# Performance work log

Hardware: AMD Instinct MI355X
Metric: run time of the kernel (lower is better)

Reference implementation:

```python
import jax, jax.numpy as jnp
import numpy as np

HEADS = 8
DIM = 512
DIM_HEAD = 64          # dim // 8
LANDMARKS = 256        # dim // 2
PINV_ITERS = 6
KSIZE = 33             # residual depthwise conv kernel (lucidrains default)
LN_EPS = 1e-5


def setup_inputs() -> dict:
    key = jax.random.key(0)
    ks = jax.random.split(key, 5)
    b, n, d = 4, 4096, DIM
    inner = HEADS * DIM_HEAD  # 512
    x = jax.random.normal(ks[0], (b, n, d), jnp.float32)
    w_qkv = jax.random.normal(ks[1], (d, inner * 3), jnp.float32) * 0.02   # to_qkv (no bias)
    w_out = jax.random.normal(ks[2], (inner, d), jnp.float32) * 0.02      # to_out linear
    b_out = jnp.zeros((d,), jnp.float32)
    res_kernel = jax.random.normal(ks[3], (HEADS, 1, KSIZE, 1), jnp.float32) * 0.02  # depthwise Conv2d, groups=heads, no bias
    gamma = jnp.ones((d,), jnp.float32)
    beta = jnp.zeros((d,), jnp.float32)
    return dict(x=x, w_qkv=w_qkv, w_out=w_out, b_out=b_out,
                res_kernel=res_kernel, gamma=gamma, beta=beta)


def _moore_penrose_pinv(mat, iters):
    # Faithful to lucidrains moore_penrose_iter_pinv: global-max scaling init.
    abs_m = jnp.abs(mat)
    col = abs_m.sum(-1)
    row = abs_m.sum(-2)
    z = jnp.swapaxes(mat, -1, -2) / (jnp.max(col) * jnp.max(row))
    eye = jnp.eye(mat.shape[-1], dtype=mat.dtype)
    for _ in range(iters):
        mz = mat @ z
        z = 0.25 * z @ (13.0 * eye - mz @ (15.0 * eye - mz @ (7.0 * eye - mz)))
    return z


def reference(x, w_qkv, w_out, b_out, res_kernel, gamma, beta):
    b, n, d = x.shape
    # --- pre-norm (torch LayerNorm: biased variance) ---
    mu = x.mean(-1, keepdims=True)
    var = ((x - mu) ** 2).mean(-1, keepdims=True)
    xn = (x - mu) / jnp.sqrt(var + LN_EPS) * gamma + beta

    # --- qkv ---
    qkv = xn @ w_qkv                                     # [b, n, 3*inner]
    q, k, v = jnp.split(qkv, 3, axis=-1)
    split = lambda t: t.reshape(b, n, HEADS, DIM_HEAD).transpose(0, 2, 1, 3)  # [b,h,n,d]
    q, k, v = split(q), split(k), split(v)
    q = q * (DIM_HEAD ** -0.5)

    # --- landmarks (n divisible by LANDMARKS: no padding branch) ---
    m = LANDMARKS
    l = n // m
    q_l = q.reshape(b, HEADS, m, l, DIM_HEAD).mean(3)    # [b,h,m,d]
    k_l = k.reshape(b, HEADS, m, l, DIM_HEAD).mean(3)

    attn1 = jax.nn.softmax(jnp.einsum('bhid,bhjd->bhij', q, k_l), axis=-1)   # [b,h,n,m]
    attn2 = jax.nn.softmax(jnp.einsum('bhid,bhjd->bhij', q_l, k_l), axis=-1) # [b,h,m,m]
    attn3 = jax.nn.softmax(jnp.einsum('bhid,bhjd->bhij', q_l, k), axis=-1)   # [b,h,m,n]
    attn2_inv = _moore_penrose_pinv(attn2, PINV_ITERS)

    out = (attn1 @ attn2_inv) @ (attn3 @ v)              # [b,h,n,d]

    # --- depthwise conv residual over sequence dim (groups=heads) ---
    pad = KSIZE // 2
    res = jax.lax.conv_general_dilated(
        v, res_kernel, window_strides=(1, 1), padding=((pad, pad), (0, 0)),
        dimension_numbers=('NCHW', 'OIHW', 'NCHW'), feature_group_count=HEADS)
    out = out + res

    # --- merge heads, output proj (dropout = identity at inference) ---
    out = out.transpose(0, 2, 1, 3).reshape(b, n, HEADS * DIM_HEAD)
    out = out @ w_out + b_out

    # --- outer residual ---
    return x + out
```

## Files before the change

kernel.cpp:

```cpp
#include <hip/hip_runtime.h>
#include <stdint.h>

#define DEV __device__ __forceinline__

typedef unsigned short u16;
typedef unsigned int u32;
using f32x4 = __attribute__((ext_vector_type(4))) float;
using u32x4 = __attribute__((ext_vector_type(4))) u32;
using bf16x8 = __attribute__((ext_vector_type(8))) __bf16;

DEV float b2f(u16 u) { u32 x = ((u32)u) << 16; return __builtin_bit_cast(float, x); }
DEV u16 f2b(float f) {
  u32 x = __builtin_bit_cast(u32, f);
  return (u16)((x + 0x7FFFu + ((x >> 16) & 1u)) >> 16);
}
DEV u32 pk2(float a, float b) { return (u32)f2b(a) | ((u32)f2b(b) << 16); }
DEV bf16x8 lds_frag(const u16* p) { return __builtin_bit_cast(bf16x8, *(const u32x4*)p); }
DEV bf16x8 g_frag(const u16* p) { return __builtin_bit_cast(bf16x8, *(const u32x4*)p); }
DEV f32x4 mfma16(bf16x8 a, bf16x8 b, f32x4 c) {
  return __builtin_amdgcn_mfma_f32_16x16x32_bf16(a, b, c, 0, 0, 0);
}
DEV float wredmax(float v) {
#pragma unroll
  for (int m = 32; m > 0; m >>= 1) v = fmaxf(v, __shfl_xor(v, m));
  return v;
}
DEV float wredsum(float v) {
#pragma unroll
  for (int m = 32; m > 0; m >>= 1) v += __shfl_xor(v, m);
  return v;
}

__global__ __launch_bounds__(256) void ln_k(const float* __restrict__ x,
                                            const float* __restrict__ gamma,
                                            const float* __restrict__ beta,
                                            u16* __restrict__ xn) {
  int row = blockIdx.x, tid = threadIdx.x;
  int lane = tid & 63, wave = tid >> 6;
  const float* xr = x + (size_t)row * 512;
  float a = xr[2 * tid], b = xr[2 * tid + 1];
  __shared__ float red[8];
  float s = wredsum(a + b);
  if (lane == 0) red[wave] = s;
  __syncthreads();
  float mean = (red[0] + red[1] + red[2] + red[3]) * (1.0f / 512.0f);
  float da = a - mean, db = b - mean;
  float vs = wredsum(da * da + db * db);
  if (lane == 0) red[4 + wave] = vs;
  __syncthreads();
  float var = (red[4] + red[5] + red[6] + red[7]) * (1.0f / 512.0f);
  float rstd = rsqrtf(var + 1e-5f);
  int c = 2 * tid;
  u16 o0 = f2b(da * rstd * gamma[c] + beta[c]);
  u16 o1 = f2b(db * rstd * gamma[c + 1] + beta[c + 1]);
  *(u32*)&xn[(size_t)row * 512 + c] = (u32)o0 | ((u32)o1 << 16);
}

__global__ __launch_bounds__(256) void transpose_w(const float* __restrict__ in,
                                                   u16* __restrict__ out, int R, int C) {
  __shared__ float t[64][65];
  int c0 = blockIdx.x * 64, r0 = blockIdx.y * 64;
  int tid = threadIdx.x;
  int r = tid >> 2, cs = (tid & 3) * 16;
  const float* src = in + (size_t)(r0 + r) * C + c0 + cs;
#pragma unroll
  for (int e = 0; e < 16; e++) t[r][cs + e] = src[e];
  __syncthreads();
  int c = tid >> 2, rs = (tid & 3) * 16;
  u16* dst = out + (size_t)(c0 + c) * R + r0 + rs;
#pragma unroll
  for (int e = 0; e < 16; e++) dst[e] = f2b(t[rs + e][c]);
}

__global__ __launch_bounds__(256) void transpose_k(const u16* __restrict__ k,
                                                   u16* __restrict__ kT) {
  __shared__ u16 t[64][72];
  int bh = blockIdx.y, i0 = blockIdx.x * 64;
  int tid = threadIdx.x;
  int r = tid >> 2, ds = (tid & 3) * 16;
  const u16* src = k + (((size_t)bh * 4096) + i0 + r) * 64 + ds;
#pragma unroll
  for (int e = 0; e < 16; e++) t[r][ds + e] = src[e];
  __syncthreads();
  int d = tid >> 2, is = (tid & 3) * 16;
  u16* dst = kT + ((size_t)bh * 64 + d) * 4096 + i0 + is;
#pragma unroll
  for (int e = 0; e < 16; e++) dst[e] = t[is + e][d];
}

__global__ __launch_bounds__(256) void landmark_mean(const u16* __restrict__ src,
                                                     u16* __restrict__ dh,
                                                     u16* __restrict__ dl,
                                                     u16* __restrict__ dF) {
  int gid = blockIdx.x * 4 + (threadIdx.x >> 6);
  int lane = threadIdx.x & 63;
  int bh = gid >> 8, lm = gid & 255;
  const u16* p = src + (((size_t)bh * 4096) + lm * 16) * 64 + lane;
  float s = 0.f;
#pragma unroll
  for (int t = 0; t < 16; t++) s += b2f(p[t * 64]);
  float m = s * (1.0f / 16.0f);
  u16 hi = f2b(m);
  size_t idx = ((size_t)bh * 256 + lm) * 64 + lane;
  dh[idx] = hi;
  dl[idx] = f2b(m - b2f(hi));
  if (dF) {
    size_t a = ((((size_t)bh * 16 + (lm >> 4)) * 2 + (lane >> 5)) * 512) +
               (((lane >> 3) & 3) * 128) + ((lm & 15) * 8) + (lane & 7);
    dF[a] = hi;
  }
}

template <int MODE>
__global__ __launch_bounds__(256) void gemm_bf16_nt(
    const u16* __restrict__ A, const u16* __restrict__ Bt, int K,
    u16* __restrict__ oq, u16* __restrict__ ok, u16* __restrict__ ov,
    const float* __restrict__ xres, const float* __restrict__ bias,
    float* __restrict__ oc) {
  constexpr int BM = 128, BN = 128, BK = 32, LDT = BK + 8;
  constexpr int SMEM = (MODE == 1) ? (128 * 132 * 4) : (128 * 136 * 2);
  __shared__ __align__(16) char smem[SMEM];
  u16(*Al)[LDT] = (u16(*)[LDT])smem;
  u16(*Bl)[LDT] = (u16(*)[LDT])(smem + BM * LDT * 2);
  int tid = threadIdx.x;
  int lane = tid & 63, wave = tid >> 6;
  int bm = blockIdx.x * BM, bn = blockIdx.y * BN;
  int wm = (wave >> 1) * 64, wn = (wave & 1) * 64;
  f32x4 acc[4][4] = {};
  for (int kt = 0; kt < K; kt += BK) {
    __syncthreads();
#pragma unroll
    for (int c = 0; c < 2; c++) {
      int chunk = tid + c * 256;
      int r = chunk >> 2, kc = (chunk & 3) * 8;
      const u16* src;
      if (MODE == 0) {
        src = A + (size_t)(bm + r) * K + kt + kc;
      } else {
        int m = bm + r, kk = kt + kc;
        src = A + ((((size_t)(m >> 12)) * 8 + (kk >> 6)) * 4096 + (m & 4095)) * 64 + (kk & 63);
      }
      *(u32x4*)&Al[r][kc] = *(const u32x4*)src;
      const u16* srcb = Bt + (size_t)(bn + r) * K + kt + kc;
      *(u32x4*)&Bl[r][kc] = *(const u32x4*)srcb;
    }
    __syncthreads();
    bf16x8 af[4], bf_[4];
#pragma unroll
    for (int i = 0; i < 4; i++) af[i] = lds_frag(&Al[wm + i * 16 + (lane & 15)][8 * (lane >> 4)]);
#pragma unroll
    for (int i = 0; i < 4; i++) bf_[i] = lds_frag(&Bl[wn + i * 16 + (lane & 15)][8 * (lane >> 4)]);
#pragma unroll
    for (int mi = 0; mi < 4; mi++)
#pragma unroll
      for (int ni = 0; ni < 4; ni++) acc[mi][ni] = mfma16(af[mi], bf_[ni], acc[mi][ni]);
  }
  __syncthreads();
  if (MODE == 0) {
    u16(*Cl)[136] = (u16(*)[136])smem;
    int tensor = bn / 512;
    float scale = (tensor == 0) ? 0.125f : 1.0f;
#pragma unroll
    for (int mi = 0; mi < 4; mi++)
      for (int ni = 0; ni < 4; ni++)
        for (int r = 0; r < 4; r++) {
          int row = wm + mi * 16 + 4 * (lane >> 4) + r;
          int col = wn + ni * 16 + (lane & 15);
          Cl[row][col] = f2b(acc[mi][ni][r] * scale);
        }
    __syncthreads();
    int half = tid >> 7, r = tid & 127;
    int m = bm + r, b = m >> 12, i = m & 4095;
    int cw = (bn % 512) + half * 64;
    int h = cw >> 6;
    u16* base = (tensor == 0) ? oq : (tensor == 1 ? ok : ov);
    u16* dst = base + (((size_t)(b * 8 + h)) * 4096 + i) * 64;
#pragma unroll
    for (int j = 0; j < 64; j += 8) *(u32x4*)(dst + j) = *(const u32x4*)&Cl[r][half * 64 + j];
  } else {
    float(*Cf)[132] = (float(*)[132])smem;
#pragma unroll
    for (int mi = 0; mi < 4; mi++)
      for (int ni = 0; ni < 4; ni++)
        for (int r = 0; r < 4; r++) {
          int row = wm + mi * 16 + 4 * (lane >> 4) + r;
          int col = wn + ni * 16 + (lane & 15);
          Cf[row][col] = acc[mi][ni][r];
        }
    __syncthreads();
    int r = tid >> 1, seg = (tid & 1) * 64;
    int m = bm + r;
    const float* xr = xres + (size_t)m * 512 + bn + seg;
    const float* br = bias + bn + seg;
    float* orow = oc + (size_t)m * 512 + bn + seg;
#pragma unroll
    for (int j = 0; j < 64; j += 4) {
      f32x4 cv = *(const f32x4*)&Cf[r][seg + j];
      f32x4 xv = *(const f32x4*)&xr[j];
      f32x4 bv = *(const f32x4*)&br[j];
      cv = cv + xv + bv;
      *(f32x4*)&orow[j] = cv;
    }
  }
}

template <int OMODE, int PREC>
__global__ __launch_bounds__(256) void ns_gemm(
    const u16* __restrict__ Ahg, const u16* __restrict__ Alg,
    const u16* __restrict__ Bhg, const u16* __restrict__ Blg, int K, int sA, int sB,
    u16* __restrict__ Ch, u16* __restrict__ Cl2, u16* __restrict__ Th, u16* __restrict__ Tl,
    float* __restrict__ Cf, u16* __restrict__ Tu,
    float cC, float aC, float cT, float aT, int wrC, int wrT) {
  __shared__ __align__(16) u16 Ahs[64][72], Als[64][72], Bhs[64][72], Bls[64][72];
  int bz = blockIdx.z;
  int tid = threadIdx.x, lane = tid & 63, wave = tid >> 6;
  int l15 = lane & 15, g = lane >> 4;
  int bm = blockIdx.x * 64, bn = blockIdx.y * 64;
  int wm = (wave >> 1) * 32, wn = (wave & 1) * 32;
  const u16* Ah0 = Ahg + (size_t)bz * sA;
  const u16* Al0 = Alg + (size_t)bz * sA;
  const u16* Bh0 = Bhg + (size_t)bz * sB;
  const u16* Bl0 = Blg + (size_t)bz * sB;
  int r = tid >> 2, c16 = (tid & 3) * 16;
  const u16* pa = Ah0 + (size_t)(bm + r) * K + c16;
  const u16* pal = Al0 + (size_t)(bm + r) * K + c16;
  const u16* pb = Bh0 + (size_t)(bn + r) * K + c16;
  const u16* pbl = Bl0 + (size_t)(bn + r) * K + c16;
  u32x4 ra0 = *(const u32x4*)pa, ra1 = *(const u32x4*)(pa + 8);
  u32x4 rc0 = *(const u32x4*)pb, rc1 = *(const u32x4*)(pb + 8);
  u32x4 rb0, rb1, rd0, rd1;
  if (PREC) {
    rb0 = *(const u32x4*)pal;
    rb1 = *(const u32x4*)(pal + 8);
    rd0 = *(const u32x4*)pbl;
    rd1 = *(const u32x4*)(pbl + 8);
  }
  f32x4 acc[2][2] = {};
  int nt = K >> 6;
  for (int t = 0; t < nt; t++) {
    __syncthreads();
    *(u32x4*)&Ahs[r][c16] = ra0;
    *(u32x4*)&Ahs[r][c16 + 8] = ra1;
    *(u32x4*)&Bhs[r][c16] = rc0;
    *(u32x4*)&Bhs[r][c16 + 8] = rc1;
    if (PREC) {
      *(u32x4*)&Als[r][c16] = rb0;
      *(u32x4*)&Als[r][c16 + 8] = rb1;
      *(u32x4*)&Bls[r][c16] = rd0;
      *(u32x4*)&Bls[r][c16 + 8] = rd1;
    }
    __syncthreads();
    if (t + 1 < nt) {
      int kt = (t + 1) << 6;
      ra0 = *(const u32x4*)(pa + kt);
      ra1 = *(const u32x4*)(pa + kt + 8);
      rc0 = *(const u32x4*)(pb + kt);
      rc1 = *(const u32x4*)(pb + kt + 8);
      if (PREC) {
        rb0 = *(const u32x4*)(pal + kt);
        rb1 = *(const u32x4*)(pal + kt + 8);
        rd0 = *(const u32x4*)(pbl + kt);
        rd1 = *(const u32x4*)(pbl + kt + 8);
      }
    }
#pragma unroll
    for (int ks = 0; ks < 2; ks++) {
      int ko = ks * 32 + 8 * g;
      bf16x8 ah[2], al[2], bh_[2], bl_[2];
#pragma unroll
      for (int i = 0; i < 2; i++) {
        int ro = wm + i * 16 + l15;
        int rn = wn + i * 16 + l15;
        ah[i] = lds_frag(&Ahs[ro][ko]);
        bh_[i] = lds_frag(&Bhs[rn][ko]);
        if (PREC) {
          al[i] = lds_frag(&Als[ro][ko]);
          bl_[i] = lds_frag(&Bls[rn][ko]);
        }
      }
#pragma unroll
      for (int mi = 0; mi < 2; mi++)
#pragma unroll
        for (int ni = 0; ni < 2; ni++) {
          acc[mi][ni] = mfma16(ah[mi], bh_[ni], acc[mi][ni]);
          if (PREC) {
            acc[mi][ni] = mfma16(ah[mi], bl_[ni], acc[mi][ni]);
            acc[mi][ni] = mfma16(al[mi], bh_[ni], acc[mi][ni]);
          }
        }
    }
  }
#pragma unroll
  for (int mi = 0; mi < 2; mi++)
#pragma unroll
    for (int ni = 0; ni < 2; ni++) {
      int r0 = bm + wm + mi * 16 + 4 * g;
      int cg = bn + wn + ni * 16 + l15;
      f32x4 a = acc[mi][ni];
      if (OMODE == 1) {
        float* c = Cf + (size_t)bz * 65536;
#pragma unroll
        for (int rr = 0; rr < 4; rr++)
          c[(size_t)(r0 + rr) * 256 + cg] = aC * a[rr] + ((r0 + rr) == cg ? cC : 0.f);
      } else if (OMODE == 2) {
        u16 pp[4];
#pragma unroll
        for (int rr = 0; rr < 4; rr++) pp[rr] = f2b(aT * a[rr]);
        u16* tp = Tu + ((((size_t)bz * 4 + (cg >> 4)) * 8 + (r0 >> 5)) * 512) +
                  (((r0 >> 3) & 3) * 128) + ((cg & 15) * 8) + (r0 & 7);
        *(u32*)tp = (u32)pp[0] | ((u32)pp[1] << 16);
        *(u32*)(tp + 2) = (u32)pp[2] | ((u32)pp[3] << 16);
      } else {
        if (wrC) {
#pragma unroll
          for (int rr = 0; rr < 4; rr++) {
            float v = aC * a[rr] + ((r0 + rr) == cg ? cC : 0.f);
            u16 hi = f2b(v);
            size_t idx = (size_t)bz * 65536 + (size_t)(r0 + rr) * 256 + cg;
            Ch[idx] = hi;
            Cl2[idx] = f2b(v - b2f(hi));
          }
        }
        if (wrT) {
          u16 ph[4], pl[4];
#pragma unroll
          for (int rr = 0; rr < 4; rr++) {
            float v = aT * a[rr] + ((r0 + rr) == cg ? cT : 0.f);
            ph[rr] = f2b(v);
            pl[rr] = f2b(v - b2f(ph[rr]));
          }
          size_t idx = (size_t)bz * 65536 + (size_t)cg * 256 + r0;
          *(u32*)&Th[idx] = (u32)ph[0] | ((u32)ph[1] << 16);
          *(u32*)&Th[idx + 2] = (u32)ph[2] | ((u32)ph[3] << 16);
          *(u32*)&Tl[idx] = (u32)pl[0] | ((u32)pl[1] << 16);
          *(u32*)&Tl[idx + 2] = (u32)pl[2] | ((u32)pl[3] << 16);
        }
      }
    }
}

__global__ __launch_bounds__(256) void softmax256(float* __restrict__ S,
                                                  u16* __restrict__ Sh,
                                                  u16* __restrict__ Sl) {
  int row = blockIdx.x * 4 + (threadIdx.x >> 6);
  int lane = threadIdx.x & 63;
  float* r = S + (size_t)row * 256;
  f32x4 vv = *(f32x4*)&r[lane * 4];
  float mx = wredmax(fmaxf(fmaxf(vv[0], vv[1]), fmaxf(vv[2], vv[3])));
  vv[0] = __expf(vv[0] - mx);
  vv[1] = __expf(vv[1] - mx);
  vv[2] = __expf(vv[2] - mx);
  vv[3] = __expf(vv[3] - mx);
  float sm = wredsum(vv[0] + vv[1] + vv[2] + vv[3]);
  vv *= (1.0f / sm);
  *(f32x4*)&r[lane * 4] = vv;
  u16 h[4], l[4];
#pragma unroll
  for (int e = 0; e < 4; e++) {
    h[e] = f2b(vv[e]);
    l[e] = f2b(vv[e] - b2f(h[e]));
  }
  size_t p = (size_t)row * 256 + lane * 4;
  *(u32*)&Sh[p] = (u32)h[0] | ((u32)h[1] << 16);
  *(u32*)&Sh[p + 2] = (u32)h[2] | ((u32)h[3] << 16);
  *(u32*)&Sl[p] = (u32)l[0] | ((u32)l[1] << 16);
  *(u32*)&Sl[p + 2] = (u32)l[2] | ((u32)l[3] << 16);
}

__global__ __launch_bounds__(256) void pinv_part(const float* __restrict__ mat,
                                                 float* __restrict__ colpart,
                                                 float* __restrict__ scal) {
  int blk = blockIdx.x;
  int bh = blk >> 3, ch = blk & 7;
  const float* m = mat + (size_t)bh * 65536 + (size_t)ch * 32 * 256;
  int tid = threadIdx.x, lane = tid & 63, wv = tid >> 6;
  float cp = 0.f;
#pragma unroll 4
  for (int r2 = 0; r2 < 32; r2++) cp += m[r2 * 256 + tid];
  colpart[(size_t)blk * 256 + tid] = cp;
  float rmax = 0.f;
#pragma unroll
  for (int rr = 0; rr < 8; rr++) {
    f32x4 v = *(const f32x4*)&m[(wv * 8 + rr) * 256 + lane * 4];
    float s = wredsum(v[0] + v[1] + v[2] + v[3]);
    rmax = fmaxf(rmax, s);
  }
  if (lane == 0) atomicMax((int*)&scal[1], __float_as_int(rmax));
}

__global__ __launch_bounds__(256) void pinv_fin(const float* __restrict__ colpart,
                                                float* __restrict__ scal) {
  int tid = threadIdx.x;
  float mx = 0.f;
  for (int bh = 0; bh < 32; bh++) {
    float s = 0.f;
#pragma unroll
    for (int ch = 0; ch < 8; ch++) s += colpart[((size_t)bh * 8 + ch) * 256 + tid];
    mx = fmaxf(mx, s);
  }
  mx = wredmax(mx);
  __shared__ float red[4];
  if ((tid & 63) == 0) red[tid >> 6] = mx;
  __syncthreads();
  if (tid == 0) {
    float a = fmaxf(fmaxf(red[0], red[1]), fmaxf(red[2], red[3]));
    atomicMax((int*)&scal[0], __float_as_int(a));
  }
}

__global__ __launch_bounds__(256) void pinv_init(const float* __restrict__ mat,
                                                 const float* __restrict__ scal,
                                                 u16* __restrict__ zh, u16* __restrict__ zl,
                                                 u16* __restrict__ zth, u16* __restrict__ ztl) {
  size_t idx = (size_t)blockIdx.x * 256 + threadIdx.x;
  int bh = (int)(idx >> 16);
  int i = (int)((idx >> 8) & 255), j = (int)(idx & 255);
  float s = 1.0f / (scal[0] * scal[1]);
  float val = mat[idx] * s;
  u16 hi = f2b(val);
  u16 lo = f2b(val - b2f(hi));
  zth[idx] = hi;
  ztl[idx] = lo;
  size_t tixd = ((size_t)bh << 16) + ((size_t)j << 8) + i;
  zh[tixd] = hi;
  zl[tixd] = lo;
}

__global__ __launch_bounds__(512) void attn3_split(const u16* __restrict__ qlh,
                                                   const u16* __restrict__ k,
                                                   const u16* __restrict__ vT,
                                                   float* __restrict__ pacc,
                                                   float* __restrict__ ml) {
  __shared__ __align__(16) u16 kb[64][72];
  __shared__ __align__(16) u16 vtb[64][72];
  __shared__ __align__(16) u16 Pb[8][16][72];
  int tid = threadIdx.x, lane = tid & 63, wv = tid >> 6;
  int l15 = lane & 15, g = lane >> 4;
  int bh = blockIdx.y, kvc = blockIdx.x;
  const u16* kb_g = k + ((size_t)bh * 4096 + (size_t)kvc * 512) * 64;
  const u16* vb_g = vT + (size_t)bh * 64 * 4096 + (size_t)kvc * 512;
  bf16x8 aq[2][2];
#pragma unroll
  for (int ss = 0; ss < 2; ss++) {
    const u16* qlp = qlh + ((size_t)bh * 256 + wv * 32 + ss * 16 + l15) * 64 + 8 * g;
    aq[ss][0] = g_frag(qlp);
    aq[ss][1] = g_frag(qlp + 32);
  }
  int sr = tid >> 3, sc = (tid & 7) * 8;
  u32x4 rk = *(const u32x4*)(kb_g + (size_t)sr * 64 + sc);
  u32x4 rv = *(const u32x4*)(vb_g + (size_t)sr * 4096 + sc);
  f32x4 minit = {-1e30f, -1e30f, -1e30f, -1e30f};
  f32x4 mreg[2] = {minit, minit};
  f32x4 lreg[2] = {};
  f32x4 oacc[2][4] = {};
  for (int t = 0; t < 8; t++) {
    __syncthreads();
    *(u32x4*)&kb[sr][sc] = rk;
    *(u32x4*)&vtb[sr][sc] = rv;
    __syncthreads();
    if (t < 7) {
      rk = *(const u32x4*)(kb_g + (size_t)(t + 1) * 4096 + (size_t)sr * 64 + sc);
      rv = *(const u32x4*)(vb_g + (size_t)(t + 1) * 64 + (size_t)sr * 4096 + sc);
    }
#pragma unroll
    for (int ss = 0; ss < 2; ss++) {
      f32x4 sa[4] = {};
#pragma unroll
      for (int nf = 0; nf < 4; nf++) {
        bf16x8 b0 = lds_frag(&kb[nf * 16 + l15][8 * g]);
        bf16x8 b1 = lds_frag(&kb[nf * 16 + l15][8 * g + 32]);
        sa[nf] = mfma16(aq[ss][0], b0, sa[nf]);
        sa[nf] = mfma16(aq[ss][1], b1, sa[nf]);
      }
      f32x4 mn, corr;
#pragma unroll
      for (int r = 0; r < 4; r++) {
        float m_ = fmaxf(fmaxf(sa[0][r], sa[1][r]), fmaxf(sa[2][r], sa[3][r]));
#pragma unroll
        for (int msk = 1; msk < 16; msk <<= 1) m_ = fmaxf(m_, __shfl_xor(m_, msk));
        mn[r] = fmaxf(mreg[ss][r], m_);
        corr[r] = __expf(mreg[ss][r] - mn[r]);
        mreg[ss][r] = mn[r];
      }
      f32x4 ps = {};
#pragma unroll
      for (int nf = 0; nf < 4; nf++)
#pragma unroll
        for (int r = 0; r < 4; r++) {
          sa[nf][r] = __expf(sa[nf][r] - mn[r]);
          ps[r] += sa[nf][r];
        }
#pragma unroll
      for (int r = 0; r < 4; r++) {
#pragma unroll
        for (int msk = 1; msk < 16; msk <<= 1) ps[r] += __shfl_xor(ps[r], msk);
        lreg[ss][r] = lreg[ss][r] * corr[r] + ps[r];
      }
#pragma unroll
      for (int nf = 0; nf < 4; nf++) oacc[ss][nf] *= corr;
#pragma unroll
      for (int nf = 0; nf < 4; nf++)
#pragma unroll
        for (int r = 0; r < 4; r++)
          Pb[wv][4 * g + r][nf * 16 + l15] = f2b(sa[nf][r]);
      asm volatile("s_waitcnt lgkmcnt(0)" ::: "memory");
      __builtin_amdgcn_sched_barrier(0);
      bf16x8 ap0 = lds_frag(&Pb[wv][l15][8 * g]);
      bf16x8 ap1 = lds_frag(&Pb[wv][l15][8 * g + 32]);
#pragma unroll
      for (int nf = 0; nf < 4; nf++) {
        bf16x8 b0 = lds_frag(&vtb[nf * 16 + l15][8 * g]);
        bf16x8 b1 = lds_frag(&vtb[nf * 16 + l15][8 * g + 32]);
        oacc[ss][nf] = mfma16(ap0, b0, oacc[ss][nf]);
        oacc[ss][nf] = mfma16(ap1, b1, oacc[ss][nf]);
      }
    }
  }
  size_t pb = (size_t)(bh * 8 + kvc) * 64;
#pragma unroll
  for (int ss = 0; ss < 2; ss++) {
    int qbase = wv * 32 + ss * 16;
#pragma unroll
    for (int nf = 0; nf < 4; nf++)
      *(f32x4*)&pacc[(pb + nf * 16 + l15) * 256 + qbase + 4 * g] = oacc[ss][nf];
    if (l15 == 0) {
#pragma unroll
      for (int r = 0; r < 4; r++) {
        size_t mi = ((size_t)(bh * 8 + kvc) * 256 + qbase + 4 * g + r) * 2;
        ml[mi] = mreg[ss][r];
        ml[mi + 1] = lreg[ss][r];
      }
    }
  }
}

__global__ __launch_bounds__(256) void attn3_fin(const float* __restrict__ pacc,
                                                 const float* __restrict__ ml,
                                                 u16* __restrict__ w3h,
                                                 u16* __restrict__ w3l) {
  int dc = blockIdx.x, bh = blockIdx.y;
  int i = threadIdx.x;
  float m[8], l[8], w[8];
  float M = -1e30f;
#pragma unroll
  for (int kv = 0; kv < 8; kv++) {
    size_t mi = ((size_t)(bh * 8 + kv) * 256 + i) * 2;
    m[kv] = ml[mi];
    l[kv] = ml[mi + 1];
    M = fmaxf(M, m[kv]);
  }
  float den = 0.f;
#pragma unroll
  for (int kv = 0; kv < 8; kv++) {
    w[kv] = __expf(m[kv] - M);
    den += w[kv] * l[kv];
  }
  float inv = 1.0f / den;
#pragma unroll
  for (int dd = 0; dd < 16; dd++) {
    int d = dc * 16 + dd;
    float num = 0.f;
#pragma unroll
    for (int kv = 0; kv < 8; kv++)
      num += w[kv] * pacc[((size_t)(bh * 8 + kv) * 64 + d) * 256 + i];
    float val = num * inv;
    u16 hi = f2b(val);
    size_t o = ((size_t)bh * 64 + d) * 256 + i;
    w3h[o] = hi;
    w3l[o] = f2b(val - b2f(hi));
  }
}

__global__ __launch_bounds__(256, 4) void attn1_mfma(const u16* __restrict__ q,
                                                     const u16* __restrict__ kF,
                                                     const u16* __restrict__ zwF,
                                                     const u16* __restrict__ vT,
                                                     const float* __restrict__ rker,
                                                     u16* __restrict__ out_h) {
  __shared__ __align__(16) u16 Pl[64][258];
  int tid = threadIdx.x, lane = tid & 63, wv = tid >> 6;
  int l15 = lane & 15, g = lane >> 4;
  int bh = blockIdx.y, h = bh & 7;
  int i0 = blockIdx.x * 64;
  const u16* qp = q + ((size_t)bh * 4096 + i0 + wv * 16 + l15) * 64 + 8 * g;
  bf16x8 aq0 = __builtin_bit_cast(bf16x8, *(const u32x4*)qp);
  bf16x8 aq1 = __builtin_bit_cast(bf16x8, *(const u32x4*)(qp + 32));
  u16 kb16 = (lane < 33) ? f2b(rker[h * 33 + lane]) : (u16)0;
  const u16* kfb = kF + (size_t)bh * 16384 + (size_t)lane * 8;
  f32x4 sacc[16] = {};
#pragma unroll
  for (int nf = 0; nf < 16; nf++) {
    bf16x8 b0 = g_frag(kfb + (nf * 2 + 0) * 512);
    bf16x8 b1 = g_frag(kfb + (nf * 2 + 1) * 512);
    sacc[nf] = mfma16(aq0, b0, sacc[nf]);
    sacc[nf] = mfma16(aq1, b1, sacc[nf]);
  }
  bf16x8 band[2];
#pragma unroll
  for (int ks = 0; ks < 2; ks++) {
    u16 bb[8];
#pragma unroll
    for (int j = 0; j < 8; j++) {
      int idx = 32 * ks + 8 * g + j - l15;
      u16 vsh = (u16)__shfl((int)kb16, idx & 63);
      bb[j] = (idx >= 0 && idx <= 32) ? vsh : (u16)0;
    }
    band[ks] = __builtin_bit_cast(bf16x8, *(u32x4*)bb);
  }
  f32x4 cacc[4] = {};
#pragma unroll
  for (int nf = 0; nf < 4; nf++) {
    int d = nf * 16 + l15;
    const u16* vp = vT + ((size_t)bh * 64 + d) * 4096;
#pragma unroll
    for (int ks = 0; ks < 2; ks++) {
      int col0 = i0 - 16 + 16 * wv + 32 * ks + 8 * g;
      bf16x8 vf;
      if (col0 >= 0 && col0 + 7 < 4096) {
        vf = g_frag(vp + col0);
      } else {
        u16 tmp[8];
#pragma unroll
        for (int j = 0; j < 8; j++) {
          int c = col0 + j;
          tmp[j] = (c >= 0 && c < 4096) ? vp[c] : (u16)0;
        }
        vf = __builtin_bit_cast(bf16x8, *(u32x4*)tmp);
      }
      cacc[nf] = mfma16(band[ks], vf, cacc[nf]);
    }
  }
  f32x4 mx;
#pragma unroll
  for (int r = 0; r < 4; r++) {
    float m_ = sacc[0][r];
#pragma unroll
    for (int nf = 1; nf < 16; nf++) m_ = fmaxf(m_, sacc[nf][r]);
#pragma unroll
    for (int msk = 1; msk < 16; msk <<= 1) m_ = fmaxf(m_, __shfl_xor(m_, msk));
    mx[r] = m_;
  }
  f32x4 ls = {};
#pragma unroll
  for (int nf = 0; nf < 16; nf++)
#pragma unroll
    for (int r = 0; r < 4; r++) {
      sacc[nf][r] = __expf(sacc[nf][r] - mx[r]);
      ls[r] += sacc[nf][r];
    }
  f32x4 invl;
#pragma unroll
  for (int r = 0; r < 4; r++) {
#pragma unroll
    for (int msk = 1; msk < 16; msk <<= 1) ls[r] += __shfl_xor(ls[r], msk);
    invl[r] = 1.0f / ls[r];
  }
#pragma unroll
  for (int nf = 0; nf < 16; nf++)
#pragma unroll
    for (int r = 0; r < 4; r++) Pl[wv * 16 + 4 * g + r][nf * 16 + l15] = f2b(sacc[nf][r]);
  asm volatile("s_waitcnt lgkmcnt(0)" ::: "memory");
  __builtin_amdgcn_sched_barrier(0);
  bf16x8 ap[8];
#pragma unroll
  for (int ks = 0; ks < 8; ks++) ap[ks] = lds_frag(&Pl[wv * 16 + l15][8 * g + 32 * ks]);
  const u16* zfb = zwF + (size_t)bh * 16384 + (size_t)lane * 8;
  f32x4 oacc[4] = {};
#pragma unroll
  for (int nf = 0; nf < 4; nf++) {
#pragma unroll
    for (int ks = 0; ks < 8; ks++) {
      bf16x8 b = g_frag(zfb + (nf * 8 + ks) * 512);
      oacc[nf] = mfma16(ap[ks], b, oacc[nf]);
    }
  }
#pragma unroll
  for (int nf = 0; nf < 4; nf++) {
    int colc = nf * 16 + l15;
#pragma unroll
    for (int r = 0; r < 4; r++) {
      float val = oacc[nf][r] * invl[r] + cacc[nf][r];
      out_h[((size_t)bh * 4096 + i0 + wv * 16 + 4 * g + r) * 64 + colc] = f2b(val);
    }
  }
}

extern "C" void kernel_launch(void* const* d_in, const int* in_sizes, int n_in,
                              void* d_out, int out_size, void* d_ws, size_t ws_size,
                              hipStream_t stream) {
  (void)in_sizes; (void)n_in; (void)out_size;
  const float* x = (const float*)d_in[0];
  const float* w_qkv = (const float*)d_in[1];
  const float* w_out = (const float*)d_in[2];
  const float* b_out = (const float*)d_in[3];
  const float* res_k = (const float*)d_in[4];
  const float* gamma = (const float*)d_in[5];
  const float* beta = (const float*)d_in[6];
  float* out = (float*)d_out;

  char* p = (char*)d_ws;
  auto alloc = [&](size_t bytes) {
    char* r = p;
    p += (bytes + 255) & ~(size_t)255;
    return r;
  };
  const size_t BH = 32;
  const size_t PLANE = BH * 65536 * 2;
  const size_t SMALL = BH * 256 * 64 * 2;
  u16* xn = (u16*)alloc(BH * 4096 * 64 * 2);
  u16* vT = xn;
  u16* wTq = (u16*)alloc(1536 * 512 * 2);
  u16* wTo = (u16*)alloc(512 * 512 * 2);
  u16* q = (u16*)alloc(BH * 4096 * 64 * 2);
  u16* k = (u16*)alloc(BH * 4096 * 64 * 2);
  u16* v = (u16*)alloc(BH * 4096 * 64 * 2);
  u16* qlh = (u16*)alloc(SMALL);
  u16* qll = (u16*)alloc(SMALL);
  u16* klh = (u16*)alloc(SMALL);
  u16* kll = (u16*)alloc(SMALL);
  u16* kF = (u16*)alloc(SMALL);
  float* mat = (float*)alloc(BH * 65536 * 4);
  u16* t4h = (u16*)mat;
  u16* t4l = t4h + BH * 65536;
  u16* math_ = (u16*)alloc(PLANE);
  u16* matl = (u16*)alloc(PLANE);
  u16* zh = (u16*)alloc(PLANE);
  u16* zl = (u16*)alloc(PLANE);
  u16* zth = (u16*)alloc(PLANE);
  u16* ztl = (u16*)alloc(PLANE);
  char* slotB = alloc(4 * PLANE);
  u16* mzh = (u16*)slotB;
  u16* mzl = mzh + BH * 65536;
  u16* s2h = mzl + BH * 65536;
  u16* s2l = s2h + BH * 65536;
  u16* out_h = (u16*)slotB;
  u16* t3h = (u16*)alloc(PLANE);
  u16* t3l = (u16*)alloc(PLANE);
  u16* znh = (u16*)alloc(PLANE);
  u16* znl = (u16*)alloc(PLANE);
  u16* znth = (u16*)alloc(PLANE);
  u16* zntl = (u16*)alloc(PLANE);
  u16* w3h = (u16*)alloc(BH * 64 * 256 * 2);
  u16* w3l = (u16*)alloc(BH * 64 * 256 * 2);
  u16* zwF = (u16*)alloc(BH * 64 * 256 * 2);
  float* colpart = (float*)alloc(256 * 256 * 4);
  float* scal = (float*)alloc(256);
  if ((size_t)(p - (char*)d_ws) > ws_size) return;
  float* pacc = (float*)t3h;
  float* mlbuf = (float*)znth;

  hipMemsetAsync(scal, 0, 8, stream);
  ln_k<<<16384, 256, 0, stream>>>(x, gamma, beta, xn);
  transpose_w<<<dim3(24, 8), 256, 0, stream>>>(w_qkv, wTq, 512, 1536);
  transpose_w<<<dim3(8, 8), 256, 0, stream>>>(w_out, wTo, 512, 512);
  gemm_bf16_nt<0><<<dim3(128, 12), 256, 0, stream>>>(xn, wTq, 512, q, k, v, nullptr,
                                                     nullptr, nullptr);
  landmark_mean<<<2048, 256, 0, stream>>>(q, qlh, qll, nullptr);
  landmark_mean<<<2048, 256, 0, stream>>>(k, klh, kll, kF);
  transpose_k<<<dim3(64, 32), 256, 0, stream>>>(v, vT);
  ns_gemm<1, 1><<<dim3(4, 4, 32), 256, 0, stream>>>(
      qlh, qll, klh, kll, 64, 16384, 16384,
      nullptr, nullptr, nullptr, nullptr, mat, nullptr, 0.f, 1.f, 0.f, 0.f, 0, 0);
  softmax256<<<2048, 256, 0, stream>>>(mat, math_, matl);
  pinv_part<<<256, 256, 0, stream>>>(mat, colpart, scal);
  pinv_fin<<<1, 256, 0, stream>>>(colpart, scal);
  pinv_init<<<8192, 256, 0, stream>>>(mat, scal, zh, zl, zth, ztl);
  u16 *zch = zh, *zcl = zl, *zcth = zth, *zctl = ztl;
  u16 *znh_ = znh, *znl_ = znl, *znth_ = znth, *zntl_ = zntl;
  for (int it = 0; it < 6; it++) {
    dim3 g44(4, 4, 32);
    if (it < 5) {
      ns_gemm<0, 0><<<g44, 256, 0, stream>>>(
          math_, matl, zcth, zctl, 256, 65536, 65536,
          mzh, mzl, s2h, s2l, nullptr, nullptr, 0.f, 1.f, 7.f, -1.f, 1, 1);
      ns_gemm<0, 0><<<g44, 256, 0, stream>>>(
          mzh, mzl, s2h, s2l, 256, 65536, 65536,
          nullptr, nullptr, t3h, t3l, nullptr, nullptr, 0.f, 0.f, 15.f, -1.f, 0, 1);
      ns_gemm<0, 0><<<g44, 256, 0, stream>>>(
          mzh, mzl, t3h, t3l, 256, 65536, 65536,
          nullptr, nullptr, t4h, t4l, nullptr, nullptr, 0.f, 0.f, 13.f, -1.f, 0, 1);
      ns_gemm<0, 0><<<g44, 256, 0, stream>>>(
          zch, zcl, t4h, t4l, 256, 65536, 65536,
          znh_, znl_, znth_, zntl_, nullptr, nullptr, 0.f, 0.25f, 0.f, 0.25f, 1, 1);
    } else {
      ns_gemm<0, 1><<<g44, 256, 0, stream>>>(
          math_, matl, zcth, zctl, 256, 65536, 65536,
          mzh, mzl, s2h, s2l, nullptr, nullptr, 0.f, 1.f, 7.f, -1.f, 1, 1);
      ns_gemm<0, 1><<<g44, 256, 0, stream>>>(
          mzh, mzl, s2h, s2l, 256, 65536, 65536,
          nullptr, nullptr, t3h, t3l, nullptr, nullptr, 0.f, 0.f, 15.f, -1.f, 0, 1);
      ns_gemm<0, 1><<<g44, 256, 0, stream>>>(
          mzh, mzl, t3h, t3l, 256, 65536, 65536,
          nullptr, nullptr, t4h, t4l, nullptr, nullptr, 0.f, 0.f, 13.f, -1.f, 0, 1);
      ns_gemm<0, 1><<<g44, 256, 0, stream>>>(
          zch, zcl, t4h, t4l, 256, 65536, 65536,
          znh_, znl_, znth_, zntl_, nullptr, nullptr, 0.f, 0.25f, 0.f, 0.25f, 1, 1);
    }
    u16* t;
    t = zch; zch = znh_; znh_ = t;
    t = zcl; zcl = znl_; znl_ = t;
    t = zcth; zcth = znth_; znth_ = t;
    t = zctl; zctl = zntl_; zntl_ = t;
  }
  attn3_split<<<dim3(8, 32), 512, 0, stream>>>(qlh, k, vT, pacc, mlbuf);
  attn3_fin<<<dim3(4, 32), 256, 0, stream>>>(pacc, mlbuf, w3h, w3l);
  ns_gemm<2, 1><<<dim3(4, 1, 32), 256, 0, stream>>>(
      zch, zcl, w3h, w3l, 256, 65536, 16384,
      nullptr, nullptr, nullptr, nullptr, nullptr, zwF, 0.f, 0.f, 0.f, 1.f, 0, 0);
  attn1_mfma<<<dim3(64, 32), 256, 0, stream>>>(q, kF, zwF, vT, res_k, out_h);
  gemm_bf16_nt<1><<<dim3(128, 4), 256, 0, stream>>>(out_h, wTo, 512, nullptr, nullptr,
                                                    nullptr, x, b_out, out);
}
```

Baseline: 510.8 us.

## Fuse Newton-Schulz pseudo-inverse iterations into one cooperative kernel with grid syncs

Replaces the 24 separate ns_gemm launches of the six pinv iterations with a single cooperative kernel that runs all GEMM stages and uses grid.sync between dependent stages. The goal is to remove per-launch overhead and launch gaps on small 512-block GEMMs. The trade-offs are grid-wide barrier cost, precision selected at runtime instead of by template, and a residency requirement of 512 blocks of 256 threads with about 37KB LDS each. After six swaps the final z is back in zh/zl, so the downstream gemm now reads zh/zl.

```diff
diff --git a/kernel.cpp b/kernel.cpp
--- a/kernel.cpp
+++ b/kernel.cpp
@@ -1,5 +1,8 @@
 #include <hip/hip_runtime.h>
+#include <hip/hip_cooperative_groups.h>
 #include <stdint.h>
+
+namespace cg = cooperative_groups;
 
 #define DEV __device__ __forceinline__
 
@@ -204,31 +207,171 @@
   }
 }
 
+DEV void ns_body(const u16* Ahg, const u16* Alg, const u16* Bhg, const u16* Blg,
+                 int prec, u16* Ch, u16* Cl2, u16* Th, u16* Tl,
+                 float cC, float aC, float cT, float aT, int wrC, int wrT,
+                 u16 (*Ahs)[72], u16 (*Als)[72], u16 (*Bhs)[72], u16 (*Bls)[72]) {
+  const int K = 256;
+  int bz = blockIdx.z;
+  int tid = threadIdx.x, lane = tid & 63, wave = tid >> 6;
+  int l15 = lane & 15, g = lane >> 4;
+  int bm = blockIdx.x * 64, bn = blockIdx.y * 64;
+  int wm = (wave >> 1) * 32, wn = (wave & 1) * 32;
+  int r = tid >> 2, c16 = (tid & 3) * 16;
+  const u16* pa = Ahg + (size_t)bz * 65536 + (size_t)(bm + r) * K + c16;
+  const u16* pal = Alg + (size_t)bz * 65536 + (size_t)(bm + r) * K + c16;
+  const u16* pb = Bhg + (size_t)bz * 65536 + (size_t)(bn + r) * K + c16;
+  const u16* pbl = Blg + (size_t)bz * 65536 + (size_t)(bn + r) * K + c16;
+  u32x4 ra0 = *(const u32x4*)pa, ra1 = *(const u32x4*)(pa + 8);
+  u32x4 rc0 = *(const u32x4*)pb, rc1 = *(const u32x4*)(pb + 8);
+  u32x4 rb0 = {}, rb1 = {}, rd0 = {}, rd1 = {};
+  if (prec) {
+    rb0 = *(const u32x4*)pal;
+    rb1 = *(const u32x4*)(pal + 8);
+    rd0 = *(const u32x4*)pbl;
+    rd1 = *(const u32x4*)(pbl + 8);
+  }
+  f32x4 acc[2][2] = {};
+  const int nt = 4;
+  for (int t = 0; t < nt; t++) {
+    __syncthreads();
+    *(u32x4*)&Ahs[r][c16] = ra0;
+    *(u32x4*)&Ahs[r][c16 + 8] = ra1;
+    *(u32x4*)&Bhs[r][c16] = rc0;
+    *(u32x4*)&Bhs[r][c16 + 8] = rc1;
+    if (prec) {
+      *(u32x4*)&Als[r][c16] = rb0;
+      *(u32x4*)&Als[r][c16 + 8] = rb1;
+      *(u32x4*)&Bls[r][c16] = rd0;
+      *(u32x4*)&Bls[r][c16 + 8] = rd1;
+    }
+    __syncthreads();
+    if (t + 1 < nt) {
+      int kt = (t + 1) << 6;
+      ra0 = *(const u32x4*)(pa + kt);
+      ra1 = *(const u32x4*)(pa + kt + 8);
+      rc0 = *(const u32x4*)(pb + kt);
+      rc1 = *(const u32x4*)(pb + kt + 8);
+      if (prec) {
+        rb0 = *(const u32x4*)(pal + kt);
+        rb1 = *(const u32x4*)(pal + kt + 8);
+        rd0 = *(const u32x4*)(pbl + kt);
+        rd1 = *(const u32x4*)(pbl + kt + 8);
+      }
+    }
+#pragma unroll
+    for (int ks = 0; ks < 2; ks++) {
+      int ko = ks * 32 + 8 * g;
+      bf16x8 ah[2], al[2], bh_[2], bl_[2];
+#pragma unroll
+      for (int i = 0; i < 2; i++) {
+        int ro = wm + i * 16 + l15;
+        int rn = wn + i * 16 + l15;
+        ah[i] = lds_frag(&Ahs[ro][ko]);
+        bh_[i] = lds_frag(&Bhs[rn][ko]);
+        if (prec) {
+          al[i] = lds_frag(&Als[ro][ko]);
+          bl_[i] = lds_frag(&Bls[rn][ko]);
+        }
+      }
+#pragma unroll
+      for (int mi = 0; mi < 2; mi++)
+#pragma unroll
+        for (int ni = 0; ni < 2; ni++) {
+          acc[mi][ni] = mfma16(ah[mi], bh_[ni], acc[mi][ni]);
+          if (prec) {
+            acc[mi][ni] = mfma16(ah[mi], bl_[ni], acc[mi][ni]);
+            acc[mi][ni] = mfma16(al[mi], bh_[ni], acc[mi][ni]);
+          }
+        }
+    }
+  }
+#pragma unroll
+  for (int mi = 0; mi < 2; mi++)
+#pragma unroll
+    for (int ni = 0; ni < 2; ni++) {
+      int r0 = bm + wm + mi * 16 + 4 * g;
+      int cg = bn + wn + ni * 16 + l15;
+      f32x4 a = acc[mi][ni];
+      if (wrC) {
+#pragma unroll
+        for (int rr = 0; rr < 4; rr++) {
+          float v = aC * a[rr] + ((r0 + rr) == cg ? cC : 0.f);
+          u16 hi = f2b(v);
+          size_t idx = (size_t)bz * 65536 + (size_t)(r0 + rr) * 256 + cg;
+          Ch[idx] = hi;
+          Cl2[idx] = f2b(v - b2f(hi));
+        }
+      }
+      if (wrT) {
+        u16 ph[4], pl[4];
+#pragma unroll
+        for (int rr = 0; rr < 4; rr++) {
+          float v = aT * a[rr] + ((r0 + rr) == cg ? cT : 0.f);
+          ph[rr] = f2b(v);
+          pl[rr] = f2b(v - b2f(ph[rr]));
+        }
+        size_t idx = (size_t)bz * 65536 + (size_t)cg * 256 + r0;
+        *(u32*)&Th[idx] = (u32)ph[0] | ((u32)ph[1] << 16);
+        *(u32*)&Th[idx + 2] = (u32)ph[2] | ((u32)ph[3] << 16);
+        *(u32*)&Tl[idx] = (u32)pl[0] | ((u32)pl[1] << 16);
+        *(u32*)&Tl[idx + 2] = (u32)pl[2] | ((u32)pl[3] << 16);
+      }
+    }
+}
+
+__global__ __launch_bounds__(256) void ns_chain(
+    const u16* math_, const u16* matl,
+    u16* zh, u16* zl, u16* zth, u16* ztl,
+    u16* mzh, u16* mzl, u16* s2h, u16* s2l,
+    u16* t3h, u16* t3l, u16* t4h, u16* t4l,
+    u16* znh, u16* znl, u16* znth, u16* zntl) {
+  __shared__ __align__(16) u16 Ahs[64][72], Als[64][72], Bhs[64][72], Bls[64][72];
+  cg::grid_group grid = cg::this_grid();
+  u16 *zch = zh, *zcl = zl, *zcth = zth, *zctl = ztl;
+  u16 *znh_ = znh, *znl_ = znl, *znth_ = znth, *zntl_ = zntl;
+  for (int it = 0; it < 6; it++) {
+    int prec = (it == 5) ? 1 : 0;
+    ns_body(math_, matl, zcth, zctl, prec, mzh, mzl, s2h, s2l,
+            0.f, 1.f, 7.f, -1.f, 1, 1, Ahs, Als, Bhs, Bls);
+    grid.sync();
+    ns_body(mzh, mzl, s2h, s2l, prec, nullptr, nullptr, t3h, t3l,
+            0.f, 0.f, 15.f, -1.f, 0, 1, Ahs, Als, Bhs, Bls);
+    grid.sync();
+    ns_body(mzh, mzl, t3h, t3l, prec, nullptr, nullptr, t4h, t4l,
+            0.f, 0.f, 13.f, -1.f, 0, 1, Ahs, Als, Bhs, Bls);
+    grid.sync();
+    ns_body(zch, zcl, t4h, t4l, prec, znh_, znl_, znth_, zntl_,
+            0.f, 0.25f, 0.f, 0.25f, 1, 1, Ahs, Als, Bhs, Bls);
+    if (it < 5) grid.sync();
+    u16* t;
+    t = zch; zch = znh_; znh_ = t;
+    t = zcl; zcl = znl_; znl_ = t;
+    t = zcth; zcth = znth_; znth_ = t;
+    t = zctl; zctl = zntl_; zntl_ = t;
+  }
+}
+
 template <int OMODE, int PREC>
 __global__ __launch_bounds__(256) void ns_gemm(
     const u16* __restrict__ Ahg, const u16* __restrict__ Alg,
     const u16* __restrict__ Bhg, const u16* __restrict__ Blg, int K, int sA, int sB,
-    u16* __restrict__ Ch, u16* __restrict__ Cl2, u16* __restrict__ Th, u16* __restrict__ Tl,
-    float* __restrict__ Cf, u16* __restrict__ Tu,
-    float cC, float aC, float cT, float aT, int wrC, int wrT) {
+    float* __restrict__ Cf, u16* __restrict__ Tu, float cC, float aC, float aT) {
   __shared__ __align__(16) u16 Ahs[64][72], Als[64][72], Bhs[64][72], Bls[64][72];
   int bz = blockIdx.z;
   int tid = threadIdx.x, lane = tid & 63, wave = tid >> 6;
   int l15 = lane & 15, g = lane >> 4;
   int bm = blockIdx.x * 64, bn = blockIdx.y * 64;
   int wm = (wave >> 1) * 32, wn = (wave & 1) * 32;
-  const u16* Ah0 = Ahg + (size_t)bz * sA;
-  const u16* Al0 = Alg + (size_t)bz * sA;
-  const u16* Bh0 = Bhg + (size_t)bz * sB;
-  const u16* Bl0 = Blg + (size_t)bz * sB;
   int r = tid >> 2, c16 = (tid & 3) * 16;
-  const u16* pa = Ah0 + (size_t)(bm + r) * K + c16;
-  const u16* pal = Al0 + (size_t)(bm + r) * K + c16;
-  const u16* pb = Bh0 + (size_t)(bn + r) * K + c16;
-  const u16* pbl = Bl0 + (size_t)(bn + r) * K + c16;
+  const u16* pa = Ahg + (size_t)bz * sA + (size_t)(bm + r) * K + c16;
+  const u16* pal = Alg + (size_t)bz * sA + (size_t)(bm + r) * K + c16;
+  const u16* pb = Bhg + (size_t)bz * sB + (size_t)(bn + r) * K + c16;
+  const u16* pbl = Blg + (size_t)bz * sB + (size_t)(bn + r) * K + c16;
+  int nt = K >> 6;
   u32x4 ra0 = *(const u32x4*)pa, ra1 = *(const u32x4*)(pa + 8);
   u32x4 rc0 = *(const u32x4*)pb, rc1 = *(const u32x4*)(pb + 8);
-  u32x4 rb0, rb1, rd0, rd1;
+  u32x4 rb0 = {}, rb1 = {}, rd0 = {}, rd1 = {};
   if (PREC) {
     rb0 = *(const u32x4*)pal;
     rb1 = *(const u32x4*)(pal + 8);
@@ -236,7 +379,6 @@
     rd1 = *(const u32x4*)(pbl + 8);
   }
   f32x4 acc[2][2] = {};
-  int nt = K >> 6;
   for (int t = 0; t < nt; t++) {
     __syncthreads();
     *(u32x4*)&Ahs[r][c16] = ra0;
@@ -302,7 +444,7 @@
 #pragma unroll
         for (int rr = 0; rr < 4; rr++)
           c[(size_t)(r0 + rr) * 256 + cg] = aC * a[rr] + ((r0 + rr) == cg ? cC : 0.f);
-      } else if (OMODE == 2) {
+      } else {
         u16 pp[4];
 #pragma unroll
         for (int rr = 0; rr < 4; rr++) pp[rr] = f2b(aT * a[rr]);
@@ -310,31 +452,6 @@
                   (((r0 >> 3) & 3) * 128) + ((cg & 15) * 8) + (r0 & 7);
         *(u32*)tp = (u32)pp[0] | ((u32)pp[1] << 16);
         *(u32*)(tp + 2) = (u32)pp[2] | ((u32)pp[3] << 16);
-      } else {
-        if (wrC) {
-#pragma unroll
-          for (int rr = 0; rr < 4; rr++) {
-            float v = aC * a[rr] + ((r0 + rr) == cg ? cC : 0.f);
-            u16 hi = f2b(v);
-            size_t idx = (size_t)bz * 65536 + (size_t)(r0 + rr) * 256 + cg;
-            Ch[idx] = hi;
-            Cl2[idx] = f2b(v - b2f(hi));
-          }
-        }
-        if (wrT) {
-          u16 ph[4], pl[4];
-#pragma unroll
-          for (int rr = 0; rr < 4; rr++) {
-            float v = aT * a[rr] + ((r0 + rr) == cg ? cT : 0.f);
-            ph[rr] = f2b(v);
-            pl[rr] = f2b(v - b2f(ph[rr]));
-          }
-          size_t idx = (size_t)bz * 65536 + (size_t)cg * 256 + r0;
-          *(u32*)&Th[idx] = (u32)ph[0] | ((u32)ph[1] << 16);
-          *(u32*)&Th[idx + 2] = (u32)ph[2] | ((u32)ph[3] << 16);
-          *(u32*)&Tl[idx] = (u32)pl[0] | ((u32)pl[1] << 16);
-          *(u32*)&Tl[idx + 2] = (u32)pl[2] | ((u32)pl[3] << 16);
-        }
       }
     }
 }
@@ -759,54 +876,24 @@
   landmark_mean<<<2048, 256, 0, stream>>>(k, klh, kll, kF);
   transpose_k<<<dim3(64, 32), 256, 0, stream>>>(v, vT);
   ns_gemm<1, 1><<<dim3(4, 4, 32), 256, 0, stream>>>(
-      qlh, qll, klh, kll, 64, 16384, 16384,
-      nullptr, nullptr, nullptr, nullptr, mat, nullptr, 0.f, 1.f, 0.f, 0.f, 0, 0);
+      qlh, qll, klh, kll, 64, 16384, 16384, mat, nullptr, 0.f, 1.f, 0.f);
   softmax256<<<2048, 256, 0, stream>>>(mat, math_, matl);
   pinv_part<<<256, 256, 0, stream>>>(mat, colpart, scal);
   pinv_fin<<<1, 256, 0, stream>>>(colpart, scal);
   pinv_init<<<8192, 256, 0, stream>>>(mat, scal, zh, zl, zth, ztl);
-  u16 *zch = zh, *zcl = zl, *zcth = zth, *zctl = ztl;
-  u16 *znh_ = znh, *znl_ = znl, *znth_ = znth, *zntl_ = zntl;
-  for (int it = 0; it < 6; it++) {
-    dim3 g44(4, 4, 32);
-    if (it < 5) {
-      ns_gemm<0, 0><<<g44, 256, 0, stream>>>(
-          math_, matl, zcth, zctl, 256, 65536, 65536,
-          mzh, mzl, s2h, s2l, nullptr, nullptr, 0.f, 1.f, 7.f, -1.f, 1, 1);
-      ns_gemm<0, 0><<<g44, 256, 0, stream>>>(
-          mzh, mzl, s2h, s2l, 256, 65536, 65536,
-          nullptr, nullptr, t3h, t3l, nullptr, nullptr, 0.f, 0.f, 15.f, -1.f, 0, 1);
-      ns_gemm<0, 0><<<g44, 256, 0, stream>>>(
-          mzh, mzl, t3h, t3l, 256, 65536, 65536,
-          nullptr, nullptr, t4h, t4l, nullptr, nullptr, 0.f, 0.f, 13.f, -1.f, 0, 1);
-      ns_gemm<0, 0><<<g44, 256, 0, stream>>>(
-          zch, zcl, t4h, t4l, 256, 65536, 65536,
-          znh_, znl_, znth_, zntl_, nullptr, nullptr, 0.f, 0.25f, 0.f, 0.25f, 1, 1);
-    } else {
-      ns_gemm<0, 1><<<g44, 256, 0, stream>>>(
-          math_, matl, zcth, zctl, 256, 65536, 65536,
-          mzh, mzl, s2h, s2l, nullptr, nullptr, 0.f, 1.f, 7.f, -1.f, 1, 1);
-      ns_gemm<0, 1><<<g44, 256, 0, stream>>>(
-          mzh, mzl, s2h, s2l, 256, 65536, 65536,
-          nullptr, nullptr, t3h, t3l, nullptr, nullptr, 0.f, 0.f, 15.f, -1.f, 0, 1);
-      ns_gemm<0, 1><<<g44, 256, 0, stream>>>(
-          mzh, mzl, t3h, t3l, 256, 65536, 65536,
-          nullptr, nullptr, t4h, t4l, nullptr, nullptr, 0.f, 0.f, 13.f, -1.f, 0, 1);
-      ns_gemm<0, 1><<<g44, 256, 0, stream>>>(
-          zch, zcl, t4h, t4l, 256, 65536, 65536,
-          znh_, znl_, znth_, zntl_, nullptr, nullptr, 0.f, 0.25f, 0.f, 0.25f, 1, 1);
-    }
-    u16* t;
-    t = zch; zch = znh_; znh_ = t;
-    t = zcl; zcl = znl_; znl_ = t;
-    t = zcth; zcth = znth_; znth_ = t;
-    t = zctl; zctl = zntl_; zntl_ = t;
+  {
+    void* args[] = {(void*)&math_, (void*)&matl, (void*)&zh,   (void*)&zl,
+                    (void*)&zth,   (void*)&ztl,  (void*)&mzh,  (void*)&mzl,
+                    (void*)&s2h,   (void*)&s2l,  (void*)&t3h,  (void*)&t3l,
+                    (void*)&t4h,   (void*)&t4l,  (void*)&znh,  (void*)&znl,
+                    (void*)&znth,  (void*)&zntl};
+    hipLaunchCooperativeKernel((const void*)ns_chain, dim3(4, 4, 32), dim3(256),
+                               args, 0, stream);
   }
   attn3_split<<<dim3(8, 32), 512, 0, stream>>>(qlh, k, vT, pacc, mlbuf);
   attn3_fin<<<dim3(4, 32), 256, 0, stream>>>(pacc, mlbuf, w3h, w3l);
   ns_gemm<2, 1><<<dim3(4, 1, 32), 256, 0, stream>>>(
-      zch, zcl, w3h, w3l, 256, 65536, 16384,
-      nullptr, nullptr, nullptr, nullptr, nullptr, zwF, 0.f, 0.f, 0.f, 1.f, 0, 0);
+      zh, zl, w3h, w3l, 256, 65536, 16384, nullptr, zwF, 0.f, 0.f, 1.f);
   attn1_mfma<<<dim3(64, 32), 256, 0, stream>>>(q, kF, zwF, vT, res_k, out_h);
   gemm_bf16_nt<1><<<dim3(128, 4), 256, 0, stream>>>(out_h, wTo, 512, nullptr, nullptr,
                                                     nullptr, x, b_out, out);
```

Result: slower. 1.873 ms (+266.6%).
